# Kernel tuning notes

Hardware: AMD Instinct MI355X
Metric: run time of the kernel (lower is better)

## Reference

```python
import jax, jax.numpy as jnp
import numpy as np
import math

EMBED_DIM = 1024
N_HEADS = 16
HEAD_DIM = EMBED_DIM // N_HEADS
NUM_CLASSES = 1000


def setup_inputs() -> dict:
    key = jax.random.key(0)
    k_x, k_wi, k_bi, k_wo, k_bo = jax.random.split(key, 5)
    bs, seq_len = 2, 2048
    x = jax.random.normal(k_x, (bs, seq_len, EMBED_DIM), dtype=jnp.float32)
    # torch.nn.Linear default init: U(-1/sqrt(fan_in), 1/sqrt(fan_in))
    bi = 1.0 / math.sqrt(EMBED_DIM)
    W_in = jax.random.uniform(k_wi, (EMBED_DIM, EMBED_DIM), minval=-bi, maxval=bi, dtype=jnp.float32)
    b_in = jax.random.uniform(k_bi, (EMBED_DIM,), minval=-bi, maxval=bi, dtype=jnp.float32)
    W_out = jax.random.uniform(k_wo, (NUM_CLASSES, EMBED_DIM), minval=-bi, maxval=bi, dtype=jnp.float32)
    b_out = jax.random.uniform(k_bo, (NUM_CLASSES,), minval=-bi, maxval=bi, dtype=jnp.float32)
    return {"x": x, "W_in": W_in, "b_in": b_in, "W_out": W_out, "b_out": b_out}


def reference(x, W_in, b_in, W_out, b_out):
    bs, seq_len, f = x.shape
    # input projection: x @ W_in^T + b_in
    p = jnp.einsum('bsf,gf->bsg', x, W_in) + b_in           # [bs, seq, embed]
    p = p.reshape(bs, seq_len, N_HEADS, HEAD_DIM)            # [bs, seq, h, d]
    p = jnp.transpose(p, (0, 2, 1, 3))                        # [bs, h, seq, d]
    scale = 1.0 / math.sqrt(f)                                # note: sqrt(embed_dim), not head_dim
    attn = jnp.einsum('bhqd,bhkd->bhqk', p, p) * scale        # [bs, h, seq, seq], no softmax
    vals = jnp.einsum('bhqk,bhkd->bhqd', attn, p)             # [bs, h, seq, d]
    vals = jnp.transpose(vals, (0, 2, 1, 3)).reshape(bs, seq_len, f)
    out = jnp.einsum('bsf,cf->bsc', vals, W_out) + b_out      # [bs, seq, num_classes]
    return out
```

## Files before the change

### kernel.cpp

```cpp
#include <hip/hip_runtime.h>
#include <hip/hip_bf16.h>
#include <cstdint>

#define EMBED   1024
#define NHEADS  16
#define HDIM    64
#define SEQ     2048
#define BSZ     2
#define MTOT    (BSZ*SEQ)
#define NCLS    1000
#define NPAD    1024

typedef __attribute__((ext_vector_type(8))) short short8;
typedef __attribute__((ext_vector_type(4))) short short4v;
typedef __attribute__((ext_vector_type(4))) float float4v;

typedef __attribute__((address_space(3))) unsigned lds_uint;
typedef __attribute__((address_space(1))) const unsigned gbl_uint;

__device__ __forceinline__ void gl2lds16(const void* g, void* l) {
    __builtin_amdgcn_global_load_lds((gbl_uint*)g, (lds_uint*)l, 16, 0, 0);
}

#define WAITVM6() asm volatile("s_waitcnt vmcnt(6)" ::: "memory")
#define WAITVM0() asm volatile("s_waitcnt vmcnt(0)" ::: "memory")
#define BAR()     asm volatile("s_barrier" ::: "memory")

__device__ __forceinline__ void storeC(float* p, float v) { *p = v; }
__device__ __forceinline__ void storeC(__hip_bfloat16* p, float v) { *p = __float2bfloat16(v); }

#define XN4  ((MTOT*EMBED)/4)
#define WN4  ((EMBED*EMBED)/4)
#define GN4  (32*64*64/4)
__global__ __launch_bounds__(256)
void conv_inputs(const float* __restrict__ x, const float* __restrict__ Win,
                 __hip_bfloat16* __restrict__ xb, __hip_bfloat16* __restrict__ Winb,
                 float* __restrict__ G) {
    const long i4 = (long)blockIdx.x * 256 + threadIdx.x;
    if (i4 < GN4)
        *(float4v*)(G + i4 * 4) = (float4v){0.f, 0.f, 0.f, 0.f};
    float4v v;
    __hip_bfloat16* dst;
    if (i4 < XN4) {
        v = *(const float4v*)(x + i4 * 4);
        dst = xb + i4 * 4;
    } else {
        const long j = i4 - XN4;
        v = *(const float4v*)(Win + j * 4);
        dst = Winb + j * 4;
    }
    short4v o;
#pragma unroll
    for (int u = 0; u < 4; u++)
        ((__hip_bfloat16*)&o)[u] = __float2bfloat16(v[u]);
    *(short4v*)dst = o;
}

template <typename CT>
__global__ __launch_bounds__(256)
void gemm_bt_bias(const __hip_bfloat16* __restrict__ A,
                  const __hip_bfloat16* __restrict__ B,
                  const float* __restrict__ bias,
                  CT* __restrict__ C,
                  int K, int nstore, int cstride, long bstride) {
    __shared__ __hip_bfloat16 As[2][128 * 64];
    __shared__ __hip_bfloat16 Bs[2][64 * 64];

    const int t    = threadIdx.x;
    const int blk  = blockIdx.x;
    const int xcd  = blk & 7;
    const int j    = blk >> 3;
    const int bm   = (xcd * 4 + (j & 3)) * 128;
    const int bn   = (j >> 2) * 64;
    const __hip_bfloat16* Bb = B + (long)(bm >> 11) * bstride;
    const int wave = t >> 6, lane = t & 63;
    const int wm   = (wave & 1) * 64, wn = (wave >> 1) * 32;
    const int lrow = lane & 15, lq = lane >> 4;

    const __hip_bfloat16* Arow[4];
    const __hip_bfloat16* Brow[2];
#pragma unroll
    for (int i = 0; i < 4; i++) {
        const int ci = i * 256 + t;
        const int r  = ci >> 3;
        const int sc = ((ci & 7) ^ (r & 7)) * 8;
        Arow[i] = A + (long)(bm + r) * K + sc;
    }
#pragma unroll
    for (int i = 0; i < 2; i++) {
        const int ci = i * 256 + t;
        const int r  = ci >> 3;
        const int sc = ((ci & 7) ^ (r & 7)) * 8;
        Brow[i] = Bb + (long)(bn + r) * K + sc;
    }

    float4v acc[4][2];
#pragma unroll
    for (int i = 0; i < 4; i++)
#pragma unroll
        for (int jj = 0; jj < 2; jj++) acc[i][jj] = (float4v){0.f, 0.f, 0.f, 0.f};

    const int nIter = K >> 6;

#define STAGE_TILE(k0, buf)                                                     \
    do {                                                                        \
        _Pragma("unroll")                                                       \
        for (int i = 0; i < 4; i++)                                             \
            gl2lds16(Arow[i] + (k0), (char*)As[buf] + (i * 256 + t) * 16);      \
        _Pragma("unroll")                                                       \
        for (int i = 0; i < 2; i++)                                             \
            gl2lds16(Brow[i] + (k0), (char*)Bs[buf] + (i * 256 + t) * 16);      \
    } while (0)

    STAGE_TILE(0, 0);

    for (int it = 0; it < nIter; ++it) {
        const int cur = it & 1, nxt = cur ^ 1;
        if (it + 1 < nIter) {
            STAGE_TILE((it + 1) << 6, nxt);
            WAITVM6();
        } else {
            WAITVM0();
        }
        BAR();

        const __hip_bfloat16* Ac = As[cur];
        const __hip_bfloat16* Bc = Bs[cur];
#pragma unroll
        for (int kk = 0; kk < 2; kk++) {
            short8 af[4], bf[2];
#pragma unroll
            for (int i = 0; i < 4; i++) {
                const int row = wm + i * 16 + lrow;
                const int sc  = (kk * 4 + lq) ^ (row & 7);
                af[i] = *(const short8*)(Ac + row * 64 + sc * 8);
            }
#pragma unroll
            for (int jj = 0; jj < 2; jj++) {
                const int row = wn + jj * 16 + lrow;
                const int sc  = (kk * 4 + lq) ^ (row & 7);
                bf[jj] = *(const short8*)(Bc + row * 64 + sc * 8);
            }
#pragma unroll
            for (int i = 0; i < 4; i++)
#pragma unroll
                for (int jj = 0; jj < 2; jj++)
                    acc[i][jj] = __builtin_amdgcn_mfma_f32_16x16x32_bf16(af[i], bf[jj], acc[i][jj], 0, 0, 0);
        }
        BAR();
    }
#undef STAGE_TILE

    float bv[2];
#pragma unroll
    for (int jj = 0; jj < 2; jj++) {
        const int gn = bn + wn + jj * 16 + lrow;
        bv[jj] = (gn < nstore) ? bias[gn] : 0.f;
    }
#pragma unroll
    for (int i = 0; i < 4; i++) {
        const int gm0 = bm + wm + i * 16 + lq * 4;
#pragma unroll
        for (int jj = 0; jj < 2; jj++) {
            const int gn = bn + wn + jj * 16 + lrow;
            if (gn < nstore) {
#pragma unroll
                for (int r = 0; r < 4; r++)
                    storeC(&C[(long)(gm0 + r) * cstride + gn], acc[i][jj][r] + bv[jj]);
            }
        }
    }
}

__global__ __launch_bounds__(256)
void gram_kernel(const __hip_bfloat16* __restrict__ P, float* __restrict__ G) {
    const int bh = blockIdx.x;
    const int ck = blockIdx.y;
    const int b = bh >> 4, h = bh & 15;
    const int row0 = b * SEQ + ck * 128;

    __shared__ float Pl[128][68];
    const int t = threadIdx.x;
#pragma unroll
    for (int it = 0; it < 4; it++) {
        const int ci = it * 256 + t;
        const int r = ci >> 3, c8 = (ci & 7) * 8;
        short8 v = *(const short8*)(P + (long)(row0 + r) * EMBED + h * HDIM + c8);
        float4v f0, f1;
#pragma unroll
        for (int u = 0; u < 4; u++) {
            f0[u] = __bfloat162float(((const __hip_bfloat16*)&v)[u]);
            f1[u] = __bfloat162float(((const __hip_bfloat16*)&v)[u + 4]);
        }
        *(float4v*)&Pl[r][c8]     = f0;
        *(float4v*)&Pl[r][c8 + 4] = f1;
    }
    __syncthreads();

    const int ty = t >> 4, tx = t & 15;
    float acc[4][4] = {};
    for (int k = 0; k < 128; k++) {
        float4v a  = *(const float4v*)&Pl[k][4 * ty];
        float4v bb = *(const float4v*)&Pl[k][4 * tx];
#pragma unroll
        for (int i = 0; i < 4; i++)
#pragma unroll
            for (int j = 0; j < 4; j++) acc[i][j] += a[i] * bb[j];
    }
    float* Gh = G + bh * 4096;
#pragma unroll
    for (int i = 0; i < 4; i++)
#pragma unroll
        for (int j = 0; j < 4; j++)
            atomicAdd(&Gh[(4 * ty + i) * 64 + 4 * tx + j], acc[i][j]);
}

__global__ __launch_bounds__(256)
void weff_kernel(const float* __restrict__ Wout, const float* __restrict__ G,
                 __hip_bfloat16* __restrict__ WeffT) {
    const int n0 = blockIdx.x * 64;
    const int h  = blockIdx.y;
    const int b  = blockIdx.z;
    const float* Gh = G + (b * 16 + h) * 4096;

    __shared__ float Wl[64][65];
    __shared__ float Gl[64][64];
    const int t = threadIdx.x;

#pragma unroll
    for (int it = 0; it < 4; it++) {
        const int ci = it * 256 + t;
        const int r = ci >> 4, c4 = (ci & 15) * 4;
        const int gr = n0 + r;
        float4v v = (float4v){0.f, 0.f, 0.f, 0.f};
        if (gr < NCLS)
            v = *(const float4v*)(Wout + (long)gr * EMBED + h * HDIM + c4);
        Wl[r][c4 + 0] = v[0]; Wl[r][c4 + 1] = v[1];
        Wl[r][c4 + 2] = v[2]; Wl[r][c4 + 3] = v[3];
    }
#pragma unroll
    for (int it = 0; it < 4; it++) {
        const int ci = it * 256 + t;
        const int r = ci >> 4, c4 = (ci & 15) * 4;
        *(float4v*)&Gl[r][c4] = *(const float4v*)&Gh[r * 64 + c4];
    }
    __syncthreads();

    const int ty = t >> 4, tx = t & 15;
    float acc[4][4] = {};
    for (int k = 0; k < 64; k++) {
        const float a0 = Wl[4 * ty + 0][k];
        const float a1 = Wl[4 * ty + 1][k];
        const float a2 = Wl[4 * ty + 2][k];
        const float a3 = Wl[4 * ty + 3][k];
        float4v g = *(const float4v*)&Gl[k][4 * tx];
#pragma unroll
        for (int j = 0; j < 4; j++) {
            acc[0][j] += a0 * g[j];
            acc[1][j] += a1 * g[j];
            acc[2][j] += a2 * g[j];
            acc[3][j] += a3 * g[j];
        }
    }
    const float scale = 1.0f / 32.0f;
    __hip_bfloat16* Wt = WeffT + (long)b * EMBED * NPAD;
#pragma unroll
    for (int i = 0; i < 4; i++) {
        const int gr = n0 + 4 * ty + i;
        short4v ov;
#pragma unroll
        for (int j = 0; j < 4; j++)
            ((__hip_bfloat16*)&ov)[j] = __float2bfloat16(acc[i][j] * scale);
        *(short4v*)(Wt + (long)gr * EMBED + h * HDIM + 4 * tx) = ov;
    }
}

extern "C" void kernel_launch(void* const* d_in, const int* in_sizes, int n_in,
                              void* d_out, int out_size, void* d_ws, size_t ws_size,
                              hipStream_t stream) {
    const float* x     = (const float*)d_in[0];
    const float* W_in  = (const float*)d_in[1];
    const float* b_in  = (const float*)d_in[2];
    const float* W_out = (const float*)d_in[3];
    const float* b_out = (const float*)d_in[4];
    float* out = (float*)d_out;

    char* ws = (char*)d_ws;
    __hip_bfloat16* xb    = (__hip_bfloat16*)(ws);
    __hip_bfloat16* Winb  = (__hip_bfloat16*)(ws + (8u  << 20));
    __hip_bfloat16* P     = (__hip_bfloat16*)(ws + (10u << 20));
    float*          G     = (float*)(ws + (18u << 20));
    __hip_bfloat16* WeffT = (__hip_bfloat16*)(ws + (19u << 20));

    conv_inputs<<<(XN4 + WN4) / 256, 256, 0, stream>>>(x, W_in, xb, Winb, G);
    gemm_bt_bias<__hip_bfloat16><<<512, 256, 0, stream>>>(xb, Winb, b_in, P, EMBED, NPAD, NPAD, 0);
    gram_kernel<<<dim3(32, 16), 256, 0, stream>>>(P, G);
    weff_kernel<<<dim3(16, 16, 2), 256, 0, stream>>>(W_out, G, WeffT);
    gemm_bt_bias<float><<<512, 256, 0, stream>>>(P, WeffT, b_out, out, EMBED, NCLS, NCLS, (long)EMBED * NPAD);
}
```

Measured before the change: 152.2 us.

## Fuse five kernels into one cooperative persistent kernel with grid syncs

Replaces the five separate launches (convert, input GEMM, Gram, Weff, output GEMM) with a single cooperative kernel of 512 blocks that runs each phase in turn, separated by grid-wide syncs and thread fences. Shared memory is one 48KB buffer reused by every phase. The goal is to remove per-launch overhead and the gaps between kernels. In exchange it adds the cost of grid barriers, limits occupancy to two blocks per CU through the shared buffer size and launch bounds, and depends on the cooperative launch succeeding with all 512 blocks resident.

```diff
diff --git a/kernel.cpp b/kernel.cpp
--- a/kernel.cpp
+++ b/kernel.cpp
@@ -1,6 +1,9 @@
 #include <hip/hip_runtime.h>
 #include <hip/hip_bf16.h>
+#include <hip/hip_cooperative_groups.h>
 #include <cstdint>
+
+namespace cg = cooperative_groups;
 
 #define EMBED   1024
 #define NHEADS  16
@@ -32,42 +35,23 @@
 #define XN4  ((MTOT*EMBED)/4)
 #define WN4  ((EMBED*EMBED)/4)
 #define GN4  (32*64*64/4)
-__global__ __launch_bounds__(256)
-void conv_inputs(const float* __restrict__ x, const float* __restrict__ Win,
-                 __hip_bfloat16* __restrict__ xb, __hip_bfloat16* __restrict__ Winb,
-                 float* __restrict__ G) {
-    const long i4 = (long)blockIdx.x * 256 + threadIdx.x;
-    if (i4 < GN4)
-        *(float4v*)(G + i4 * 4) = (float4v){0.f, 0.f, 0.f, 0.f};
-    float4v v;
-    __hip_bfloat16* dst;
-    if (i4 < XN4) {
-        v = *(const float4v*)(x + i4 * 4);
-        dst = xb + i4 * 4;
-    } else {
-        const long j = i4 - XN4;
-        v = *(const float4v*)(Win + j * 4);
-        dst = Winb + j * 4;
-    }
-    short4v o;
-#pragma unroll
-    for (int u = 0; u < 4; u++)
-        ((__hip_bfloat16*)&o)[u] = __float2bfloat16(v[u]);
-    *(short4v*)dst = o;
-}
+
+struct KParams {
+    const float* x; const float* Win; const float* b_in;
+    const float* Wout; const float* b_out;
+    float* out;
+    __hip_bfloat16* xb; __hip_bfloat16* Winb; __hip_bfloat16* P; __hip_bfloat16* WeffT;
+    float* G;
+};
 
 template <typename CT>
-__global__ __launch_bounds__(256)
-void gemm_bt_bias(const __hip_bfloat16* __restrict__ A,
-                  const __hip_bfloat16* __restrict__ B,
-                  const float* __restrict__ bias,
-                  CT* __restrict__ C,
-                  int K, int nstore, int cstride, long bstride) {
-    __shared__ __hip_bfloat16 As[2][128 * 64];
-    __shared__ __hip_bfloat16 Bs[2][64 * 64];
-
-    const int t    = threadIdx.x;
-    const int blk  = blockIdx.x;
+__device__ __forceinline__ void gemm_phase(char* smem, int t, int blk,
+        const __hip_bfloat16* __restrict__ A, const __hip_bfloat16* __restrict__ B,
+        const float* __restrict__ bias, CT* __restrict__ C,
+        int K, int nstore, int cstride, long bstride) {
+    __hip_bfloat16* As = (__hip_bfloat16*)smem;
+    __hip_bfloat16* Bs = (__hip_bfloat16*)(smem + 32768);
+
     const int xcd  = blk & 7;
     const int j    = blk >> 3;
     const int bm   = (xcd * 4 + (j & 3)) * 128;
@@ -102,14 +86,14 @@
 
     const int nIter = K >> 6;
 
-#define STAGE_TILE(k0, buf)                                                     \
-    do {                                                                        \
-        _Pragma("unroll")                                                       \
-        for (int i = 0; i < 4; i++)                                             \
-            gl2lds16(Arow[i] + (k0), (char*)As[buf] + (i * 256 + t) * 16);      \
-        _Pragma("unroll")                                                       \
-        for (int i = 0; i < 2; i++)                                             \
-            gl2lds16(Brow[i] + (k0), (char*)Bs[buf] + (i * 256 + t) * 16);      \
+#define STAGE_TILE(k0, buf)                                                       \
+    do {                                                                          \
+        _Pragma("unroll")                                                         \
+        for (int i = 0; i < 4; i++)                                               \
+            gl2lds16(Arow[i] + (k0), (char*)(As + (buf) * 8192) + (i * 256 + t) * 16); \
+        _Pragma("unroll")                                                         \
+        for (int i = 0; i < 2; i++)                                               \
+            gl2lds16(Brow[i] + (k0), (char*)(Bs + (buf) * 4096) + (i * 256 + t) * 16); \
     } while (0)
 
     STAGE_TILE(0, 0);
@@ -124,8 +108,8 @@
         }
         BAR();
 
-        const __hip_bfloat16* Ac = As[cur];
-        const __hip_bfloat16* Bc = Bs[cur];
+        const __hip_bfloat16* Ac = As + cur * 8192;
+        const __hip_bfloat16* Bc = Bs + cur * 4096;
 #pragma unroll
         for (int kk = 0; kk < 2; kk++) {
             short8 af[4], bf[2];
@@ -172,15 +156,14 @@
     }
 }
 
-__global__ __launch_bounds__(256)
-void gram_kernel(const __hip_bfloat16* __restrict__ P, float* __restrict__ G) {
-    const int bh = blockIdx.x;
-    const int ck = blockIdx.y;
+__device__ __forceinline__ void gram_phase(char* smem, int t, int blk,
+        const __hip_bfloat16* __restrict__ P, float* __restrict__ G) {
+    float (*Pl)[68] = (float(*)[68])smem;
+    const int bh = blk >> 4;
+    const int ck = blk & 15;
     const int b = bh >> 4, h = bh & 15;
     const int row0 = b * SEQ + ck * 128;
 
-    __shared__ float Pl[128][68];
-    const int t = threadIdx.x;
 #pragma unroll
     for (int it = 0; it < 4; it++) {
         const int ci = it * 256 + t;
@@ -205,27 +188,25 @@
 #pragma unroll
         for (int i = 0; i < 4; i++)
 #pragma unroll
-            for (int j = 0; j < 4; j++) acc[i][j] += a[i] * bb[j];
+            for (int jj = 0; jj < 4; jj++) acc[i][jj] += a[i] * bb[jj];
     }
     float* Gh = G + bh * 4096;
 #pragma unroll
     for (int i = 0; i < 4; i++)
 #pragma unroll
-        for (int j = 0; j < 4; j++)
-            atomicAdd(&Gh[(4 * ty + i) * 64 + 4 * tx + j], acc[i][j]);
-}
-
-__global__ __launch_bounds__(256)
-void weff_kernel(const float* __restrict__ Wout, const float* __restrict__ G,
-                 __hip_bfloat16* __restrict__ WeffT) {
-    const int n0 = blockIdx.x * 64;
-    const int h  = blockIdx.y;
-    const int b  = blockIdx.z;
+        for (int jj = 0; jj < 4; jj++)
+            atomicAdd(&Gh[(4 * ty + i) * 64 + 4 * tx + jj], acc[i][jj]);
+}
+
+__device__ __forceinline__ void weff_phase(char* smem, int t, int blk,
+        const float* __restrict__ Wout, const float* __restrict__ G,
+        __hip_bfloat16* __restrict__ WeffT) {
+    float (*Wl)[65] = (float(*)[65])smem;
+    float (*Gl)[64] = (float(*)[64])(smem + 16640);
+    const int n0 = (blk & 15) * 64;
+    const int h  = (blk >> 4) & 15;
+    const int b  = blk >> 8;
     const float* Gh = G + (b * 16 + h) * 4096;
-
-    __shared__ float Wl[64][65];
-    __shared__ float Gl[64][64];
-    const int t = threadIdx.x;
 
 #pragma unroll
     for (int it = 0; it < 4; it++) {
@@ -255,11 +236,11 @@
         const float a3 = Wl[4 * ty + 3][k];
         float4v g = *(const float4v*)&Gl[k][4 * tx];
 #pragma unroll
-        for (int j = 0; j < 4; j++) {
-            acc[0][j] += a0 * g[j];
-            acc[1][j] += a1 * g[j];
-            acc[2][j] += a2 * g[j];
-            acc[3][j] += a3 * g[j];
+        for (int jj = 0; jj < 4; jj++) {
+            acc[0][jj] += a0 * g[jj];
+            acc[1][jj] += a1 * g[jj];
+            acc[2][jj] += a2 * g[jj];
+            acc[3][jj] += a3 * g[jj];
         }
     }
     const float scale = 1.0f / 32.0f;
@@ -269,32 +250,79 @@
         const int gr = n0 + 4 * ty + i;
         short4v ov;
 #pragma unroll
-        for (int j = 0; j < 4; j++)
-            ((__hip_bfloat16*)&ov)[j] = __float2bfloat16(acc[i][j] * scale);
+        for (int jj = 0; jj < 4; jj++)
+            ((__hip_bfloat16*)&ov)[jj] = __float2bfloat16(acc[i][jj] * scale);
         *(short4v*)(Wt + (long)gr * EMBED + h * HDIM + 4 * tx) = ov;
     }
+}
+
+__global__ __launch_bounds__(256, 2)
+void fused_pipeline(KParams p) {
+    __shared__ __align__(16) char smem[49152];
+    cg::grid_group grid = cg::this_grid();
+    const int t   = threadIdx.x;
+    const int blk = blockIdx.x;
+
+    {
+        const long stride = 512L * 256;
+        for (long i4 = (long)blk * 256 + t; i4 < XN4 + WN4; i4 += stride) {
+            if (i4 < GN4)
+                *(float4v*)(p.G + i4 * 4) = (float4v){0.f, 0.f, 0.f, 0.f};
+            float4v v;
+            __hip_bfloat16* dst;
+            if (i4 < XN4) {
+                v = *(const float4v*)(p.x + i4 * 4);
+                dst = p.xb + i4 * 4;
+            } else {
+                const long jj = i4 - XN4;
+                v = *(const float4v*)(p.Win + jj * 4);
+                dst = p.Winb + jj * 4;
+            }
+            short4v o;
+#pragma unroll
+            for (int u = 0; u < 4; u++)
+                ((__hip_bfloat16*)&o)[u] = __float2bfloat16(v[u]);
+            *(short4v*)dst = o;
+        }
+    }
+    __threadfence();
+    grid.sync();
+
+    gemm_phase<__hip_bfloat16>(smem, t, blk, p.xb, p.Winb, p.b_in, p.P,
+                               EMBED, NPAD, NPAD, 0);
+    __threadfence();
+    grid.sync();
+
+    gram_phase(smem, t, blk, p.P, p.G);
+    __threadfence();
+    grid.sync();
+
+    weff_phase(smem, t, blk, p.Wout, p.G, p.WeffT);
+    __threadfence();
+    grid.sync();
+
+    gemm_phase<float>(smem, t, blk, p.P, p.WeffT, p.b_out, p.out,
+                      EMBED, NCLS, NCLS, (long)EMBED * NPAD);
 }
 
 extern "C" void kernel_launch(void* const* d_in, const int* in_sizes, int n_in,
                               void* d_out, int out_size, void* d_ws, size_t ws_size,
                               hipStream_t stream) {
-    const float* x     = (const float*)d_in[0];
-    const float* W_in  = (const float*)d_in[1];
-    const float* b_in  = (const float*)d_in[2];
-    const float* W_out = (const float*)d_in[3];
-    const float* b_out = (const float*)d_in[4];
-    float* out = (float*)d_out;
-
     char* ws = (char*)d_ws;
-    __hip_bfloat16* xb    = (__hip_bfloat16*)(ws);
-    __hip_bfloat16* Winb  = (__hip_bfloat16*)(ws + (8u  << 20));
-    __hip_bfloat16* P     = (__hip_bfloat16*)(ws + (10u << 20));
-    float*          G     = (float*)(ws + (18u << 20));
-    __hip_bfloat16* WeffT = (__hip_bfloat16*)(ws + (19u << 20));
-
-    conv_inputs<<<(XN4 + WN4) / 256, 256, 0, stream>>>(x, W_in, xb, Winb, G);
-    gemm_bt_bias<__hip_bfloat16><<<512, 256, 0, stream>>>(xb, Winb, b_in, P, EMBED, NPAD, NPAD, 0);
-    gram_kernel<<<dim3(32, 16), 256, 0, stream>>>(P, G);
-    weff_kernel<<<dim3(16, 16, 2), 256, 0, stream>>>(W_out, G, WeffT);
-    gemm_bt_bias<float><<<512, 256, 0, stream>>>(P, WeffT, b_out, out, EMBED, NCLS, NCLS, (long)EMBED * NPAD);
-}
+    KParams hp;
+    hp.x     = (const float*)d_in[0];
+    hp.Win   = (const float*)d_in[1];
+    hp.b_in  = (const float*)d_in[2];
+    hp.Wout  = (const float*)d_in[3];
+    hp.b_out = (const float*)d_in[4];
+    hp.out   = (float*)d_out;
+    hp.xb    = (__hip_bfloat16*)(ws);
+    hp.Winb  = (__hip_bfloat16*)(ws + (8u  << 20));
+    hp.P     = (__hip_bfloat16*)(ws + (10u << 20));
+    hp.G     = (float*)(ws + (18u << 20));
+    hp.WeffT = (__hip_bfloat16*)(ws + (19u << 20));
+
+    void* args[] = { &hp };
+    hipLaunchCooperativeKernel((void*)fused_pipeline, dim3(512), dim3(256),
+                               args, 0, stream);
+}
```

Measured after the change: 557.0 us. 3.66x slower.

## Fuse per-head Gram computation into projection GEMM epilogue and use MFMA for Weff

Applied to the files above, without the earlier changes.

The separate gram kernel is removed. The input-projection GEMM now stages its bf16 output tile, transposed, into LDS and computes the partial P^T P with MFMA, then atomically accumulates it into G. The weff kernel moves from scalar FP32 FMAs to bf16 MFMA by converting W_out and G to bf16 in LDS. This saves one launch and one re-read of P from global memory, but G is now rounded to bf16 before the Weff product and each projection block runs a longer epilogue.

```diff
diff --git a/kernel.cpp b/kernel.cpp
--- a/kernel.cpp
+++ b/kernel.cpp
@@ -28,6 +28,19 @@
 
 __device__ __forceinline__ void storeC(float* p, float v) { *p = v; }
 __device__ __forceinline__ void storeC(__hip_bfloat16* p, float v) { *p = __float2bfloat16(v); }
+
+__device__ __forceinline__ unsigned packbf2(float a, float b) {
+    __hip_bfloat16 ha = __float2bfloat16(a), hb = __float2bfloat16(b);
+    unsigned short ua, ub;
+    __builtin_memcpy(&ua, &ha, 2); __builtin_memcpy(&ub, &hb, 2);
+    return (unsigned)ua | ((unsigned)ub << 16);
+}
+__device__ __forceinline__ short8 lds8u(const __hip_bfloat16* p) {
+    union { uint2 u[2]; short8 s; } v;
+    v.u[0] = *(const uint2*)p;
+    v.u[1] = *(const uint2*)(p + 4);
+    return v.s;
+}
 
 #define XN4  ((MTOT*EMBED)/4)
 #define WN4  ((EMBED*EMBED)/4)
@@ -56,12 +69,13 @@
     *(short4v*)dst = o;
 }
 
-template <typename CT>
+template <typename CT, bool DO_GRAM>
 __global__ __launch_bounds__(256)
 void gemm_bt_bias(const __hip_bfloat16* __restrict__ A,
                   const __hip_bfloat16* __restrict__ B,
                   const float* __restrict__ bias,
                   CT* __restrict__ C,
+                  float* __restrict__ G,
                   int K, int nstore, int cstride, long bstride) {
     __shared__ __hip_bfloat16 As[2][128 * 64];
     __shared__ __hip_bfloat16 Bs[2][64 * 64];
@@ -157,6 +171,23 @@
         const int gn = bn + wn + jj * 16 + lrow;
         bv[jj] = (gn < nstore) ? bias[gn] : 0.f;
     }
+
+    if (DO_GRAM) {
+        __hip_bfloat16* Pt = (__hip_bfloat16*)As;
+#pragma unroll
+        for (int i = 0; i < 4; i++) {
+            const int m0 = wm + i * 16 + lq * 4;
+#pragma unroll
+            for (int jj = 0; jj < 2; jj++) {
+                const int n = wn + jj * 16 + lrow;
+                unsigned* dst = (unsigned*)(Pt + n * 132 + m0);
+                dst[0] = packbf2(acc[i][jj][0] + bv[jj], acc[i][jj][1] + bv[jj]);
+                dst[1] = packbf2(acc[i][jj][2] + bv[jj], acc[i][jj][3] + bv[jj]);
+            }
+        }
+        __syncthreads();
+    }
+
 #pragma unroll
     for (int i = 0; i < 4; i++) {
         const int gm0 = bm + wm + i * 16 + lq * 4;
@@ -170,49 +201,32 @@
             }
         }
     }
-}
-
-__global__ __launch_bounds__(256)
-void gram_kernel(const __hip_bfloat16* __restrict__ P, float* __restrict__ G) {
-    const int bh = blockIdx.x;
-    const int ck = blockIdx.y;
-    const int b = bh >> 4, h = bh & 15;
-    const int row0 = b * SEQ + ck * 128;
-
-    __shared__ float Pl[128][68];
-    const int t = threadIdx.x;
-#pragma unroll
-    for (int it = 0; it < 4; it++) {
-        const int ci = it * 256 + t;
-        const int r = ci >> 3, c8 = (ci & 7) * 8;
-        short8 v = *(const short8*)(P + (long)(row0 + r) * EMBED + h * HDIM + c8);
-        float4v f0, f1;
-#pragma unroll
-        for (int u = 0; u < 4; u++) {
-            f0[u] = __bfloat162float(((const __hip_bfloat16*)&v)[u]);
-            f1[u] = __bfloat162float(((const __hip_bfloat16*)&v)[u + 4]);
-        }
-        *(float4v*)&Pl[r][c8]     = f0;
-        *(float4v*)&Pl[r][c8 + 4] = f1;
-    }
-    __syncthreads();
-
-    const int ty = t >> 4, tx = t & 15;
-    float acc[4][4] = {};
-    for (int k = 0; k < 128; k++) {
-        float4v a  = *(const float4v*)&Pl[k][4 * ty];
-        float4v bb = *(const float4v*)&Pl[k][4 * tx];
-#pragma unroll
-        for (int i = 0; i < 4; i++)
-#pragma unroll
-            for (int j = 0; j < 4; j++) acc[i][j] += a[i] * bb[j];
-    }
-    float* Gh = G + bh * 4096;
-#pragma unroll
-    for (int i = 0; i < 4; i++)
-#pragma unroll
-        for (int j = 0; j < 4; j++)
-            atomicAdd(&Gh[(4 * ty + i) * 64 + 4 * tx + j], acc[i][j]);
+
+    if (DO_GRAM) {
+        const __hip_bfloat16* Pt = (const __hip_bfloat16*)As;
+        float4v g4[4];
+#pragma unroll
+        for (int t2 = 0; t2 < 4; t2++) g4[t2] = (float4v){0.f, 0.f, 0.f, 0.f};
+        const int d1l = wave * 16 + lrow;
+#pragma unroll
+        for (int k0 = 0; k0 < 128; k0 += 32) {
+            short8 af = lds8u(Pt + d1l * 132 + k0 + lq * 8);
+#pragma unroll
+            for (int t2 = 0; t2 < 4; t2++) {
+                short8 bfr = lds8u(Pt + (t2 * 16 + lrow) * 132 + k0 + lq * 8);
+                g4[t2] = __builtin_amdgcn_mfma_f32_16x16x32_bf16(af, bfr, g4[t2], 0, 0, 0);
+            }
+        }
+        float* Gh = G + (long)((bm >> 11) * 16 + (bn >> 6)) * 4096;
+        const int d1b = wave * 16 + lq * 4;
+#pragma unroll
+        for (int t2 = 0; t2 < 4; t2++) {
+            const int d2 = t2 * 16 + lrow;
+#pragma unroll
+            for (int r = 0; r < 4; r++)
+                atomicAdd(&Gh[(d1b + r) * 64 + d2], g4[t2][r]);
+        }
+    }
 }
 
 __global__ __launch_bounds__(256)
@@ -223,55 +237,49 @@
     const int b  = blockIdx.z;
     const float* Gh = G + (b * 16 + h) * 4096;
 
-    __shared__ float Wl[64][65];
-    __shared__ float Gl[64][64];
+    __shared__ __hip_bfloat16 Wl[64 * 72];
+    __shared__ __hip_bfloat16 Gl[64 * 72];
     const int t = threadIdx.x;
 
 #pragma unroll
     for (int it = 0; it < 4; it++) {
         const int ci = it * 256 + t;
         const int r = ci >> 4, c4 = (ci & 15) * 4;
-        const int gr = n0 + r;
         float4v v = (float4v){0.f, 0.f, 0.f, 0.f};
-        if (gr < NCLS)
-            v = *(const float4v*)(Wout + (long)gr * EMBED + h * HDIM + c4);
-        Wl[r][c4 + 0] = v[0]; Wl[r][c4 + 1] = v[1];
-        Wl[r][c4 + 2] = v[2]; Wl[r][c4 + 3] = v[3];
-    }
-#pragma unroll
-    for (int it = 0; it < 4; it++) {
-        const int ci = it * 256 + t;
-        const int r = ci >> 4, c4 = (ci & 15) * 4;
-        *(float4v*)&Gl[r][c4] = *(const float4v*)&Gh[r * 64 + c4];
+        if (n0 + r < NCLS)
+            v = *(const float4v*)(Wout + (long)(n0 + r) * EMBED + h * HDIM + c4);
+        *(uint2*)(Wl + r * 72 + c4) = (uint2){packbf2(v[0], v[1]), packbf2(v[2], v[3])};
+        float4v g = *(const float4v*)(Gh + r * 64 + c4);
+        *(uint2*)(Gl + r * 72 + c4) = (uint2){packbf2(g[0], g[1]), packbf2(g[2], g[3])};
     }
     __syncthreads();
 
-    const int ty = t >> 4, tx = t & 15;
-    float acc[4][4] = {};
-    for (int k = 0; k < 64; k++) {
-        const float a0 = Wl[4 * ty + 0][k];
-        const float a1 = Wl[4 * ty + 1][k];
-        const float a2 = Wl[4 * ty + 2][k];
-        const float a3 = Wl[4 * ty + 3][k];
-        float4v g = *(const float4v*)&Gl[k][4 * tx];
-#pragma unroll
-        for (int j = 0; j < 4; j++) {
-            acc[0][j] += a0 * g[j];
-            acc[1][j] += a1 * g[j];
-            acc[2][j] += a2 * g[j];
-            acc[3][j] += a3 * g[j];
-        }
-    }
+    const int wave = t >> 6, lane = t & 63;
+    const int lrow = lane & 15, lq = lane >> 4;
+    float4v acc[4];
+#pragma unroll
+    for (int jj = 0; jj < 4; jj++) acc[jj] = (float4v){0.f, 0.f, 0.f, 0.f};
+
+#pragma unroll
+    for (int k0 = 0; k0 < 64; k0 += 32) {
+        short8 af = *(const short8*)(Wl + (wave * 16 + lrow) * 72 + k0 + lq * 8);
+#pragma unroll
+        for (int jj = 0; jj < 4; jj++) {
+            short8 bfr = *(const short8*)(Gl + (jj * 16 + lrow) * 72 + k0 + lq * 8);
+            acc[jj] = __builtin_amdgcn_mfma_f32_16x16x32_bf16(af, bfr, acc[jj], 0, 0, 0);
+        }
+    }
+
     const float scale = 1.0f / 32.0f;
     __hip_bfloat16* Wt = WeffT + (long)b * EMBED * NPAD;
 #pragma unroll
-    for (int i = 0; i < 4; i++) {
-        const int gr = n0 + 4 * ty + i;
-        short4v ov;
-#pragma unroll
-        for (int j = 0; j < 4; j++)
-            ((__hip_bfloat16*)&ov)[j] = __float2bfloat16(acc[i][j] * scale);
-        *(short4v*)(Wt + (long)gr * EMBED + h * HDIM + 4 * tx) = ov;
+    for (int jj = 0; jj < 4; jj++) {
+        const int d1 = jj * 16 + lrow;
+#pragma unroll
+        for (int r = 0; r < 4; r++) {
+            const int n = n0 + wave * 16 + lq * 4 + r;
+            Wt[(long)n * EMBED + h * HDIM + d1] = __float2bfloat16(acc[jj][r] * scale);
+        }
     }
 }
 
@@ -293,8 +301,9 @@
     __hip_bfloat16* WeffT = (__hip_bfloat16*)(ws + (19u << 20));
 
     conv_inputs<<<(XN4 + WN4) / 256, 256, 0, stream>>>(x, W_in, xb, Winb, G);
-    gemm_bt_bias<__hip_bfloat16><<<512, 256, 0, stream>>>(xb, Winb, b_in, P, EMBED, NPAD, NPAD, 0);
-    gram_kernel<<<dim3(32, 16), 256, 0, stream>>>(P, G);
+    gemm_bt_bias<__hip_bfloat16, true><<<512, 256, 0, stream>>>(
+        xb, Winb, b_in, P, G, EMBED, NPAD, NPAD, 0);
     weff_kernel<<<dim3(16, 16, 2), 256, 0, stream>>>(W_out, G, WeffT);
-    gemm_bt_bias<float><<<512, 256, 0, stream>>>(P, WeffT, b_out, out, EMBED, NCLS, NCLS, (long)EMBED * NPAD);
-}
+    gemm_bt_bias<float, false><<<512, 256, 0, stream>>>(
+        P, WeffT, b_out, out, nullptr, EMBED, NCLS, NCLS, (long)EMBED * NPAD);
+}
```

Measured after the change: 123.1 us. 1.24x faster.
